# Optimization experiments

Measured on AMD Instinct MI355X. Metric: run time of the kernel, lower is better.

Reference implementation:

```python
import jax, jax.numpy as jnp
import numpy as np

ALPHA = 1.0

def setup_inputs() -> dict:
    key = jax.random.key(0)
    k1, k2 = jax.random.split(key)
    x = jax.random.normal(k1, (65536, 256), dtype=jnp.float32)
    clusters = jax.random.normal(k2, (256, 256), dtype=jnp.float32)
    return {"x": x, "clusters": clusters}

def reference(x, clusters):
    # squared euclidean distance via the GEMM trick (same math as
    # sum((x[:,None,:] - clusters[None,:,:])**2, axis=2) without the (n,k,d) blowup)
    x2 = jnp.sum(x * x, axis=1, keepdims=True)            # [n,1]
    c2 = jnp.sum(clusters * clusters, axis=1)             # [k]
    dist2 = x2 + c2[None, :] - 2.0 * (x @ clusters.T)     # [n,k]
    q = 1.0 / (1.0 + dist2 / ALPHA)
    q = jnp.power(q, (ALPHA + 1.0) / 2.0)
    q = q / jnp.sum(q, axis=1, keepdims=True)             # row-normalize
    return q
```

## Files before the change

kernel.cpp:

```cpp
#include <hip/hip_runtime.h>


typedef float f32x4 __attribute__((ext_vector_type(4)));

#define DIM    256
#define NCLUST 256

__device__ inline int pk4_fp8(float a, float b, float c, float d) {
    int w = __builtin_amdgcn_cvt_pk_fp8_f32(a, b, 0, false);
    w = __builtin_amdgcn_cvt_pk_fp8_f32(c, d, w, true);
    return w;
}

__global__ __launch_bounds__(64) void pre_kernel(const float* __restrict__ clusters,
                                                 int* __restrict__ bfrag,
                                                 float* __restrict__ c2p1) {
    int b = blockIdx.x;
    int l = threadIdx.x;
    if (b < 128) {
        int s   = b >> 4;
        int t   = b & 15;
        int col = t * 16 + (l & 15);
        int k0  = s * 32 + (l >> 4) * 8;
        const f32x4* p = reinterpret_cast<const f32x4*>(clusters + col * DIM + k0);
        f32x4 a = p[0];
        f32x4 c = p[1];
        int lo = pk4_fp8(-2.0f * a[0], -2.0f * a[1], -2.0f * a[2], -2.0f * a[3]);
        int hi = pk4_fp8(-2.0f * c[0], -2.0f * c[1], -2.0f * c[2], -2.0f * c[3]);
        bfrag[(b * 64 + l) * 2]     = lo;
        bfrag[(b * 64 + l) * 2 + 1] = hi;
    } else {
        int j = b - 128;
        const f32x4* p = reinterpret_cast<const f32x4*>(clusters + j * DIM);
        f32x4 v = p[l];
        float s = v[0] * v[0] + v[1] * v[1] + v[2] * v[2] + v[3] * v[3];
#pragma unroll
        for (int m = 32; m >= 1; m >>= 1) s += __shfl_xor(s, m, 64);
        if (l == 0) c2p1[j] = 1.0f + s;
    }
}

__global__ __launch_bounds__(512, 2) void cluster_kernel(const float* __restrict__ x,
                                                         const f32x4* __restrict__ bfrag,
                                                         const float* __restrict__ c2p1,
                                                         float* __restrict__ out) {
    __shared__ __align__(16) char Bs[65536];

    const int tid  = threadIdx.x;
    const int lane = tid & 63;
    const int wave = tid >> 6;
    const int cl   = lane & 15;
    const int g    = lane >> 4;
    const int tile = blockIdx.x * 8 + wave;

    f32x4 ld[16];
    {
        const float* xr = x + (size_t)(tile * 16 + cl) * DIM + g * 8;
#pragma unroll
        for (int s = 0; s < 8; ++s) {
            ld[2 * s]     = *reinterpret_cast<const f32x4*>(xr + s * 32);
            ld[2 * s + 1] = *reinterpret_cast<const f32x4*>(xr + s * 32 + 4);
        }
    }

    {
        f32x4* dst = reinterpret_cast<f32x4*>(Bs);
#pragma unroll
        for (int i = 0; i < 8; ++i) {
            int idx = i * 512 + tid;
            dst[idx] = bfrag[idx];
        }
    }
    __syncthreads();

    long af[8];
    float x2p = 0.0f;
#pragma unroll
    for (int s = 0; s < 8; ++s) {
        f32x4 a = ld[2 * s], b = ld[2 * s + 1];
        x2p += a[0]*a[0] + a[1]*a[1] + a[2]*a[2] + a[3]*a[3]
             + b[0]*b[0] + b[1]*b[1] + b[2]*b[2] + b[3]*b[3];
        unsigned lo = (unsigned)pk4_fp8(a[0], a[1], a[2], a[3]);
        unsigned hi = (unsigned)pk4_fp8(b[0], b[1], b[2], b[3]);
        af[s] = (long)(((unsigned long)hi << 32) | lo);
    }
    float x2full = x2p + __shfl_xor(x2p, 16, 64);
    x2full += __shfl_xor(x2full, 32, 64);

    f32x4 acc[16];
#pragma unroll
    for (int t = 0; t < 16; ++t) {
        acc[t][0] = 0.f; acc[t][1] = 0.f; acc[t][2] = 0.f; acc[t][3] = 0.f;
    }
    const char* bsb = Bs + lane * 8;
    __builtin_amdgcn_s_setprio(1);
#pragma unroll
    for (int s = 0; s < 8; ++s) {
#pragma unroll
        for (int t = 0; t < 16; ++t) {
            long bf = *reinterpret_cast<const long*>(bsb + (s * 16 + t) * 512);
            acc[t] = __builtin_amdgcn_mfma_f32_16x16x32_fp8_fp8(
                af[s], bf, acc[t], 0, 0, 0);
        }
    }
    __builtin_amdgcn_s_setprio(0);

    float c2v[16];
#pragma unroll
    for (int t = 0; t < 16; ++t) c2v[t] = c2p1[t * 16 + cl];

    float x2j[4];
#pragma unroll
    for (int j = 0; j < 4; ++j) x2j[j] = __shfl(x2full, g * 4 + j, 64);

    float rsum[4] = {0.f, 0.f, 0.f, 0.f};
#pragma unroll
    for (int t = 0; t < 16; ++t) {
#pragma unroll
        for (int j = 0; j < 4; ++j) {
            float d = x2j[j] + c2v[t] + acc[t][j];
            float q = __builtin_amdgcn_rcpf(d);
            acc[t][j] = q;
            rsum[j] += q;
        }
    }
#pragma unroll
    for (int j = 0; j < 4; ++j) {
        float v = rsum[j];
        v += __shfl_xor(v, 1, 64); v += __shfl_xor(v, 2, 64);
        v += __shfl_xor(v, 4, 64); v += __shfl_xor(v, 8, 64);
        rsum[j] = __builtin_amdgcn_rcpf(v);
    }
    float* ob = out + (size_t)(tile * 16) * NCLUST;
#pragma unroll
    for (int t = 0; t < 16; ++t)
#pragma unroll
        for (int j = 0; j < 4; ++j)
            ob[(g * 4 + j) * NCLUST + t * 16 + cl] = acc[t][j] * rsum[j];
}

extern "C" void kernel_launch(void* const* d_in, const int* in_sizes, int n_in,
                              void* d_out, int out_size, void* d_ws, size_t ws_size,
                              hipStream_t stream) {
    const float* x        = (const float*)d_in[0];
    const float* clusters = (const float*)d_in[1];
    float* out = (float*)d_out;

    int*   bfrag = (int*)d_ws;
    float* c2p1  = (float*)((char*)d_ws + 65536);

    pre_kernel<<<384, 64, 0, stream>>>(clusters, bfrag, c2p1);

    int nrows = in_sizes[0] / DIM;
    int grid  = nrows / (8 * 16);
    cluster_kernel<<<grid, 512, 0, stream>>>(x, (const f32x4*)bfrag, c2p1, out);
}
```

Measured before the change: 31.50 us.

## Fuse cluster preprocessing into main kernel, dropping the separate pre-kernel launch

Removes the separate pre_kernel, which converted clusters to FP8 MFMA fragments and computed squared norms. Each block of the main kernel now reads the fp32 clusters directly, quantizes them into shared memory and computes the norms there, so one launch and the workspace round trip disappear. In exchange, each of the 512 blocks reads 256KB of fp32 clusters instead of 64KB of prepacked fragments and repeats the conversion arithmetic, which adds L2 traffic and prologue latency.

Measured after the change: 40.15 us. 27.4% more time.

```diff
diff --git a/kernel.cpp b/kernel.cpp
--- a/kernel.cpp
+++ b/kernel.cpp
@@ -12,39 +12,11 @@
     return w;
 }
 
-__global__ __launch_bounds__(64) void pre_kernel(const float* __restrict__ clusters,
-                                                 int* __restrict__ bfrag,
-                                                 float* __restrict__ c2p1) {
-    int b = blockIdx.x;
-    int l = threadIdx.x;
-    if (b < 128) {
-        int s   = b >> 4;
-        int t   = b & 15;
-        int col = t * 16 + (l & 15);
-        int k0  = s * 32 + (l >> 4) * 8;
-        const f32x4* p = reinterpret_cast<const f32x4*>(clusters + col * DIM + k0);
-        f32x4 a = p[0];
-        f32x4 c = p[1];
-        int lo = pk4_fp8(-2.0f * a[0], -2.0f * a[1], -2.0f * a[2], -2.0f * a[3]);
-        int hi = pk4_fp8(-2.0f * c[0], -2.0f * c[1], -2.0f * c[2], -2.0f * c[3]);
-        bfrag[(b * 64 + l) * 2]     = lo;
-        bfrag[(b * 64 + l) * 2 + 1] = hi;
-    } else {
-        int j = b - 128;
-        const f32x4* p = reinterpret_cast<const f32x4*>(clusters + j * DIM);
-        f32x4 v = p[l];
-        float s = v[0] * v[0] + v[1] * v[1] + v[2] * v[2] + v[3] * v[3];
-#pragma unroll
-        for (int m = 32; m >= 1; m >>= 1) s += __shfl_xor(s, m, 64);
-        if (l == 0) c2p1[j] = 1.0f + s;
-    }
-}
-
 __global__ __launch_bounds__(512, 2) void cluster_kernel(const float* __restrict__ x,
-                                                         const f32x4* __restrict__ bfrag,
-                                                         const float* __restrict__ c2p1,
+                                                         const float* __restrict__ clusters,
                                                          float* __restrict__ out) {
     __shared__ __align__(16) char Bs[65536];
+    __shared__ float c2s[NCLUST];
 
     const int tid  = threadIdx.x;
     const int lane = tid & 63;
@@ -63,13 +35,41 @@
         }
     }
 
-    {
-        f32x4* dst = reinterpret_cast<f32x4*>(Bs);
+    float c2a = 0.0f, c2b = 0.0f;
+#pragma unroll 1
+    for (int cc = 0; cc < 4; ++cc) {
+        f32x4 va[4], vb[4];
 #pragma unroll
-        for (int i = 0; i < 8; ++i) {
-            int idx = i * 512 + tid;
-            dst[idx] = bfrag[idx];
+        for (int u = 0; u < 4; ++u) {
+            int ui  = cc * 4 + u;
+            int t   = wave + 8 * (ui & 1);
+            int s   = ui >> 1;
+            const f32x4* p = reinterpret_cast<const f32x4*>(
+                clusters + (t * 16 + cl) * DIM + s * 32 + g * 8);
+            va[u] = p[0];
+            vb[u] = p[1];
         }
+#pragma unroll
+        for (int u = 0; u < 4; ++u) {
+            int ui  = cc * 4 + u;
+            int t   = wave + 8 * (ui & 1);
+            int s   = ui >> 1;
+            f32x4 a = va[u], b = vb[u];
+            float sq = a[0]*a[0] + a[1]*a[1] + a[2]*a[2] + a[3]*a[3]
+                     + b[0]*b[0] + b[1]*b[1] + b[2]*b[2] + b[3]*b[3];
+            if (ui & 1) c2b += sq; else c2a += sq;
+            int lo = pk4_fp8(-2.0f * a[0], -2.0f * a[1], -2.0f * a[2], -2.0f * a[3]);
+            int hi = pk4_fp8(-2.0f * b[0], -2.0f * b[1], -2.0f * b[2], -2.0f * b[3]);
+            char* dst = Bs + (size_t)((s * 16 + t) * 64 + lane) * 8;
+            *reinterpret_cast<int*>(dst)     = lo;
+            *reinterpret_cast<int*>(dst + 4) = hi;
+        }
+    }
+    c2a += __shfl_xor(c2a, 16, 64); c2a += __shfl_xor(c2a, 32, 64);
+    c2b += __shfl_xor(c2b, 16, 64); c2b += __shfl_xor(c2b, 32, 64);
+    if (g == 0) {
+        c2s[wave * 16 + cl]       = 1.0f + c2a;
+        c2s[(wave + 8) * 16 + cl] = 1.0f + c2b;
     }
     __syncthreads();
 
@@ -107,7 +107,7 @@
 
     float c2v[16];
 #pragma unroll
-    for (int t = 0; t < 16; ++t) c2v[t] = c2p1[t * 16 + cl];
+    for (int t = 0; t < 16; ++t) c2v[t] = c2s[t * 16 + cl];
 
     float x2j[4];
 #pragma unroll
@@ -146,12 +146,7 @@
     const float* clusters = (const float*)d_in[1];
     float* out = (float*)d_out;
 
-    int*   bfrag = (int*)d_ws;
-    float* c2p1  = (float*)((char*)d_ws + 65536);
-
-    pre_kernel<<<384, 64, 0, stream>>>(clusters, bfrag, c2p1);
-
     int nrows = in_sizes[0] / DIM;
     int grid  = nrows / (8 * 16);
-    cluster_kernel<<<grid, 512, 0, stream>>>(x, (const f32x4*)bfrag, c2p1, out);
+    cluster_kernel<<<grid, 512, 0, stream>>>(x, clusters, out);
 }
```
